# Performance work log

Hardware: AMD Instinct MI355X
Metric: run time of the kernel (lower is better)

Reference implementation:

```python
import jax, jax.numpy as jnp
import numpy as np

EMBED = 8192      # DYNAMIC(2048) + STATIC(6144)
U0, U1 = 1024, 256  # units
EGO = 3
NUM_HEAD = 6
ACTION = 2
MEAN_SCALE = 5.0
INIT_STD = 5.0
MIN_STD = 1e-4
BATCH = 8192


def setup_inputs() -> dict:
    key = jax.random.key(0)
    ks = jax.random.split(key, 10)
    s = lambda fan_in: 1.0 / np.sqrt(fan_in)
    x = jax.random.normal(ks[0], (BATCH, EMBED), dtype=jnp.float32)
    # command head index in [0, 6) == RoadOption.value - 1
    command = jax.random.randint(ks[1], (BATCH,), 0, NUM_HEAD, dtype=jnp.int32)
    ego_state = jax.random.normal(ks[2], (BATCH, EGO), dtype=jnp.float32)
    # shared trunk fc: Linear(EMBED -> U0)
    fc_W = jax.random.uniform(ks[3], (EMBED, U0), jnp.float32, -s(EMBED), s(EMBED))
    fc_b = jax.random.uniform(ks[4], (U0,), jnp.float32, -s(EMBED), s(EMBED))
    # per-head MLP: Linear(U0+EGO -> U1) -> ReLU -> Linear(U1 -> 2*ACTION)
    cin = U0 + EGO
    W1 = jax.random.uniform(ks[5], (NUM_HEAD, cin, U1), jnp.float32, -s(cin), s(cin))
    b1 = jax.random.uniform(ks[6], (NUM_HEAD, U1), jnp.float32, -s(cin), s(cin))
    W2 = jax.random.uniform(ks[7], (NUM_HEAD, U1, 2 * ACTION), jnp.float32, -s(U1), s(U1))
    b2 = jax.random.uniform(ks[8], (NUM_HEAD, 2 * ACTION), jnp.float32, -s(U1), s(U1))
    return {"x": x, "command": command, "ego_state": ego_state,
            "fc_W": fc_W, "fc_b": fc_b, "W1": W1, "b1": b1, "W2": W2, "b2": b2}


def reference(x, command, ego_state, fc_W, fc_b, W1, b1, W2, b2):
    # shared trunk: Linear + ReLU, then concat ego state -> [B, U0+EGO]
    h = jax.nn.relu(x @ fc_W + fc_b)
    h = jnp.concatenate([h, ego_state], axis=-1)
    # routed heads: compute all 6 small heads densely, then select per sample
    # (faithful math; an optimized kernel would gather->grouped GEMM->scatter)
    h1 = jax.nn.relu(jnp.einsum('bi,hio->bho', h, W1) + b1)          # [B, H, U1]
    h2 = jnp.einsum('bhi,hio->bho', h1, W2) + b2                      # [B, H, 2A]
    sel = jnp.take_along_axis(h2, command[:, None, None].astype(jnp.int32), axis=1)
    out = sel[:, 0, :]                                                # [B, 2A]
    mean, std = jnp.split(out, 2, axis=-1)
    mean = MEAN_SCALE * jnp.tanh(mean / MEAN_SCALE)
    raw_init_std = np.float32(np.log(np.exp(INIT_STD) - 1.0))
    std = jax.nn.softplus(std + raw_init_std) + MIN_STD
    # distribution parameters (pre TanhBijector Normal params)
    return jnp.concatenate([mean, std], axis=-1)
```

## Files before the change

### kernel.cpp

```cpp
#include <hip/hip_runtime.h>
#include <stdint.h>

typedef short bf16x8 __attribute__((ext_vector_type(8)));
typedef float f32x4 __attribute__((ext_vector_type(4)));

#define BATCH 8192
#define EMBED 8192
#define U0    1024
#define U1    256
#define NHEAD 6

__device__ __forceinline__ unsigned short f2bf(float f) {
  union { float f; unsigned int u; } v; v.f = f;
  unsigned int u = v.u;
  unsigned int r = u + 0x7FFFu + ((u >> 16) & 1u);
  return (unsigned short)(r >> 16);
}
__device__ __forceinline__ void async_copy16(const void* g, void* l) {
  __builtin_amdgcn_global_load_lds((const __attribute__((address_space(1))) void*)g,
                                   (__attribute__((address_space(3))) void*)l, 16, 0, 0);
}

__global__ void transpose_cvt_kernel(const float* __restrict__ in, unsigned short* __restrict__ out,
                                     int R, int C, long in_z, long out_z) {
  __shared__ unsigned short tile[64][65];
  const float* inp = in + (long)blockIdx.z * in_z;
  unsigned short* outp = out + (long)blockIdx.z * out_z;
  int r0 = blockIdx.x * 64;
  int c0 = blockIdx.y * 64;
  int lc = threadIdx.x & 63;
  int lr = threadIdx.x >> 6;
#pragma unroll
  for (int i = 0; i < 16; i++) {
    int r = lr + i * 4;
    tile[r][lc] = f2bf(inp[(long)(r0 + r) * C + (c0 + lc)]);
  }
  __syncthreads();
#pragma unroll
  for (int i = 0; i < 16; i++) {
    int c = lr + i * 4;
    outp[(long)(c0 + c) * R + (r0 + lc)] = tile[lc][c];
  }
}

__global__ void bucket_kernel(const int* __restrict__ cmd, int* __restrict__ idxlist,
                              int* __restrict__ meta) {
  __shared__ int cnt[NHEAD], cur[NHEAD], off[NHEAD + 1];
  int tid = threadIdx.x;
  if (tid < NHEAD) cnt[tid] = 0;
  __syncthreads();
  for (int b = tid; b < BATCH; b += blockDim.x) atomicAdd(&cnt[cmd[b]], 1);
  __syncthreads();
  if (tid == 0) {
    int s = 0;
    for (int h2 = 0; h2 < NHEAD; h2++) { off[h2] = s; s += cnt[h2]; }
    off[NHEAD] = s;
  }
  __syncthreads();
  if (tid < NHEAD) cur[tid] = off[tid];
  if (tid <= NHEAD) meta[tid] = off[tid];
  __syncthreads();
  for (int b = tid; b < BATCH; b += blockDim.x) {
    int p = atomicAdd(&cur[cmd[b]], 1);
    idxlist[p] = b;
  }
}

__global__ __launch_bounds__(256) void gemm_kernel(const float* __restrict__ x,
                                                   const unsigned short* __restrict__ wt,
                                                   float* __restrict__ pbuf) {
  __shared__ uint4 As[1024];
  __shared__ uint4 Bs[1024];
  int tid  = threadIdx.x;
  int lane = tid & 63;
  int wave = tid >> 6;
  int wm = wave >> 1, wn = wave & 1;

  int f = blockIdx.x;
  int xcd = f & 7;
  int idx = f >> 3;
  int kh  = idx >> 6;
  int sub = idx & 63;
  int by = xcd * 8 + (sub >> 3);
  int bx = sub & 7;
  int m0 = by * 128;
  int n0 = bx * 128;
  int l15 = lane & 15, lq = lane >> 4;

  long asrc[4], bsrc[4];
#pragma unroll
  for (int j = 0; j < 4; j++) {
    int c = wave * 4 + j;
    int cwm = c >> 3, cks = (c >> 2) & 1, cmi = c & 3;
    int kofs = cks * 32 + lq * 8;
    asrc[j] = (long)(m0 + cwm * 64 + cmi * 16 + l15) * EMBED + kofs;
    bsrc[j] = (long)(n0 + cwm * 64 + cmi * 16 + l15) * EMBED + kofs;
  }

  f32x4 zero = {0.f, 0.f, 0.f, 0.f};
  f32x4 acc[4][4];
#pragma unroll
  for (int mi = 0; mi < 4; mi++)
#pragma unroll
    for (int ni = 0; ni < 4; ni++) acc[mi][ni] = zero;

  const int kbeg = kh * 4096;
  for (int k0 = kbeg; k0 < kbeg + 4096; k0 += 64) {
    __syncthreads();
    float4 a0[4], a1[4];
#pragma unroll
    for (int j = 0; j < 4; j++) {
      const float* p = x + asrc[j] + k0;
      a0[j] = *(const float4*)p;
      a1[j] = *(const float4*)(p + 4);
    }
#pragma unroll
    for (int j = 0; j < 4; j++) {
      int c = wave * 4 + j;
      async_copy16(wt + bsrc[j] + k0, &Bs[c * 64 + lane]);
    }
#pragma unroll
    for (int j = 0; j < 4; j++) {
      int c = wave * 4 + j;
      unsigned int q0, q1, q2, q3;
      asm("v_cvt_pk_bf16_f32 %0, %1, %2" : "=v"(q0) : "v"(a0[j].x), "v"(a0[j].y));
      asm("v_cvt_pk_bf16_f32 %0, %1, %2" : "=v"(q1) : "v"(a0[j].z), "v"(a0[j].w));
      asm("v_cvt_pk_bf16_f32 %0, %1, %2" : "=v"(q2) : "v"(a1[j].x), "v"(a1[j].y));
      asm("v_cvt_pk_bf16_f32 %0, %1, %2" : "=v"(q3) : "v"(a1[j].z), "v"(a1[j].w));
      uint4 r; r.x = q0; r.y = q1; r.z = q2; r.w = q3;
      As[c * 64 + lane] = r;
    }
    __syncthreads();
#pragma unroll
    for (int ks = 0; ks < 2; ks++) {
      bf16x8 af[4], bfr[4];
#pragma unroll
      for (int mi = 0; mi < 4; mi++) af[mi] = *(const bf16x8*)&As[((wm * 2 + ks) * 4 + mi) * 64 + lane];
#pragma unroll
      for (int ni = 0; ni < 4; ni++) bfr[ni] = *(const bf16x8*)&Bs[((wn * 2 + ks) * 4 + ni) * 64 + lane];
#pragma unroll
      for (int mi = 0; mi < 4; mi++)
#pragma unroll
        for (int ni = 0; ni < 4; ni++)
          acc[mi][ni] = __builtin_amdgcn_mfma_f32_16x16x32_bf16(af[mi], bfr[ni], acc[mi][ni], 0, 0, 0);
    }
  }

  float* p = pbuf + (long)kh * (8192L * 1024);
#pragma unroll
  for (int ni = 0; ni < 4; ni++) {
    int col = n0 + wn * 64 + ni * 16 + l15;
#pragma unroll
    for (int mi = 0; mi < 4; mi++) {
      int rbase = m0 + wm * 64 + mi * 16 + lq * 4;
#pragma unroll
      for (int r = 0; r < 4; r++) {
        p[(long)(rbase + r) * U0 + col] = acc[mi][ni][r];
      }
    }
  }
}

__global__ __launch_bounds__(256) void reduce_kernel(const float* __restrict__ pbuf,
                                                     const float* __restrict__ fc_b,
                                                     unsigned short* __restrict__ h) {
  long i = ((long)blockIdx.x * 256 + threadIdx.x) * 8;
  const float* P1 = pbuf + 8192L * 1024;
  float4 a0 = *(const float4*)(pbuf + i);
  float4 a1 = *(const float4*)(pbuf + i + 4);
  float4 c0 = *(const float4*)(P1 + i);
  float4 c1 = *(const float4*)(P1 + i + 4);
  int cb = (int)(i & (U0 - 1));
  float4 b0 = *(const float4*)(fc_b + cb);
  float4 b1 = *(const float4*)(fc_b + cb + 4);
  float v[8];
  v[0] = a0.x + c0.x + b0.x; v[1] = a0.y + c0.y + b0.y;
  v[2] = a0.z + c0.z + b0.z; v[3] = a0.w + c0.w + b0.w;
  v[4] = a1.x + c1.x + b1.x; v[5] = a1.y + c1.y + b1.y;
  v[6] = a1.z + c1.z + b1.z; v[7] = a1.w + c1.w + b1.w;
  uint4 r;
  unsigned int q[4];
#pragma unroll
  for (int j = 0; j < 4; j++) {
    float lo = v[2 * j]     > 0.f ? v[2 * j]     : 0.f;
    float hi = v[2 * j + 1] > 0.f ? v[2 * j + 1] : 0.f;
    q[j] = (unsigned int)f2bf(lo) | ((unsigned int)f2bf(hi) << 16);
  }
  r.x = q[0]; r.y = q[1]; r.z = q[2]; r.w = q[3];
  *(uint4*)(h + i) = r;
}

__global__ __launch_bounds__(256) void head_kernel(const unsigned short* __restrict__ h,
                                                   const unsigned short* __restrict__ w1t,
                                                   const float* __restrict__ W1,
                                                   const float* __restrict__ b1,
                                                   const float* __restrict__ W2,
                                                   const float* __restrict__ b2,
                                                   const float* __restrict__ ego,
                                                   const int* __restrict__ idxlist,
                                                   const int* __restrict__ meta,
                                                   float* __restrict__ out) {
  int hd = blockIdx.y;
  int off = meta[hd];
  int cnt = meta[hd + 1] - off;
  int t0 = blockIdx.x * 32;
  if (t0 >= cnt) return;

  __shared__ int ridx[32];
  __shared__ float h1s[32][257];
  __shared__ float w2s[1024];
  int tid = threadIdx.x;
  if (tid < 32) {
    int i = t0 + tid;
    ridx[tid] = idxlist[off + (i < cnt ? i : 0)];
  }
  *(float4*)&w2s[tid * 4] = *(const float4*)(W2 + (long)hd * 1024 + tid * 4);
  __syncthreads();

  int lane = tid & 63, wave = tid >> 6;
  int l15 = lane & 15, lq = lane >> 4;

  long abase[2];
#pragma unroll
  for (int mi = 0; mi < 2; mi++) abase[mi] = (long)ridx[mi * 16 + l15] * U0 + lq * 8;
  long bbase[4];
#pragma unroll
  for (int ni = 0; ni < 4; ni++)
    bbase[ni] = (long)(hd * 256 + wave * 64 + ni * 16 + l15) * 1024 + lq * 8;

  f32x4 zero = {0.f, 0.f, 0.f, 0.f};
  f32x4 acc[2][4];
#pragma unroll
  for (int mi = 0; mi < 2; mi++)
#pragma unroll
    for (int ni = 0; ni < 4; ni++) acc[mi][ni] = zero;

#pragma unroll 2
  for (int k0 = 0; k0 < 1024; k0 += 32) {
    bf16x8 af[2], bfr[4];
#pragma unroll
    for (int mi = 0; mi < 2; mi++) af[mi] = *(const bf16x8*)(h + abase[mi] + k0);
#pragma unroll
    for (int ni = 0; ni < 4; ni++) bfr[ni] = *(const bf16x8*)(w1t + bbase[ni] + k0);
#pragma unroll
    for (int mi = 0; mi < 2; mi++)
#pragma unroll
      for (int ni = 0; ni < 4; ni++)
        acc[mi][ni] = __builtin_amdgcn_mfma_f32_16x16x32_bf16(af[mi], bfr[ni], acc[mi][ni], 0, 0, 0);
  }

  const float* W1e = W1 + (long)hd * 1027 * 256 + (long)1024 * 256;
#pragma unroll
  for (int mi = 0; mi < 2; mi++)
#pragma unroll
    for (int r = 0; r < 4; r++) {
      int rl = mi * 16 + lq * 4 + r;
      int b = ridx[rl];
      float e0 = ego[b * 3 + 0], e1 = ego[b * 3 + 1], e2 = ego[b * 3 + 2];
#pragma unroll
      for (int ni = 0; ni < 4; ni++) {
        int col = wave * 64 + ni * 16 + l15;
        float v = acc[mi][ni][r] + b1[hd * 256 + col]
                + e0 * W1e[col] + e1 * W1e[256 + col] + e2 * W1e[512 + col];
        h1s[rl][col] = v > 0.f ? v : 0.f;
      }
    }
  __syncthreads();

  if (tid < 128) {
    int t = tid >> 2, o2 = tid & 3;
    if (t0 + t < cnt) {
      float s0 = 0.f, s1 = 0.f, s2 = 0.f, s3 = 0.f;
#pragma unroll 4
      for (int i = 0; i < 256; i += 4) {
        s0 += h1s[t][i + 0] * w2s[(i + 0) * 4 + o2];
        s1 += h1s[t][i + 1] * w2s[(i + 1) * 4 + o2];
        s2 += h1s[t][i + 2] * w2s[(i + 2) * 4 + o2];
        s3 += h1s[t][i + 3] * w2s[(i + 3) * 4 + o2];
      }
      float sum = b2[hd * 4 + o2] + ((s0 + s1) + (s2 + s3));
      int b = ridx[t];
      float res;
      if (o2 < 2) {
        res = 5.0f * tanhf(sum * 0.2f);
      } else {
        float z = sum + 4.99323838f;
        res = (z > 20.f ? z : log1pf(expf(z))) + 1e-4f;
      }
      out[b * 4 + o2] = res;
    }
  }
}

extern "C" void kernel_launch(void* const* d_in, const int* in_sizes, int n_in,
                              void* d_out, int out_size, void* d_ws, size_t ws_size,
                              hipStream_t stream) {
  const float* x   = (const float*)d_in[0];
  const int*   cmd = (const int*)d_in[1];
  const float* ego = (const float*)d_in[2];
  const float* fcW = (const float*)d_in[3];
  const float* fcb = (const float*)d_in[4];
  const float* W1  = (const float*)d_in[5];
  const float* b1  = (const float*)d_in[6];
  const float* W2  = (const float*)d_in[7];
  const float* b2  = (const float*)d_in[8];
  float* out = (float*)d_out;

  char* ws = (char*)d_ws;
  float* pbuf          = (float*)(ws);
  unsigned short* wt   = (unsigned short*)(ws + 67108864);
  unsigned short* hbuf = (unsigned short*)(ws + 83886080);
  unsigned short* w1t  = (unsigned short*)(ws + 100663296);
  int* idxlist         = (int*)(ws + 103809024);
  int* meta            = (int*)(ws + 103841792);

  hipLaunchKernelGGL(transpose_cvt_kernel, dim3(128, 16, 1), dim3(256), 0, stream,
                     fcW, wt, 8192, 1024, 0L, 0L);
  hipLaunchKernelGGL(transpose_cvt_kernel, dim3(16, 4, 6), dim3(256), 0, stream,
                     W1, w1t, 1024, 256, (long)1027 * 256, (long)256 * 1024);
  hipLaunchKernelGGL(bucket_kernel, dim3(1), dim3(1024), 0, stream, cmd, idxlist, meta);
  hipLaunchKernelGGL(gemm_kernel, dim3(1024), dim3(256), 0, stream, x, wt, pbuf);
  hipLaunchKernelGGL(reduce_kernel, dim3(4096), dim3(256), 0, stream, pbuf, fcb, hbuf);
  hipLaunchKernelGGL(head_kernel, dim3(256, 6), dim3(256), 0, stream,
                     hbuf, w1t, W1, b1, W2, b2, ego, idxlist, meta, out);
}
```

Before: 788.6 us.

## Pre-convert x to bf16, drop split-K, fuse bias+ReLU epilogue into GEMM

Adds a separate pass that converts x to bf16 so the GEMM can load both operands into shared memory with async global-to-LDS copies. The split-K partial buffer and the reduce kernel are removed: each of 512 blocks of 512 threads covers the full K and applies bias, ReLU and bf16 packing in its epilogue. The bucket kernel now uses wave ballots to batch the shared-memory atomics. This trades an extra 256MB read plus 128MB write for the x conversion, and fewer blocks with twice the K loop, against removing the fp32 partial-sum traffic and the in-loop conversions.

```diff
diff --git a/kernel.cpp b/kernel.cpp
--- a/kernel.cpp
+++ b/kernel.cpp
@@ -16,9 +16,22 @@
   unsigned int r = u + 0x7FFFu + ((u >> 16) & 1u);
   return (unsigned short)(r >> 16);
 }
+__device__ __forceinline__ unsigned int pk2(float lo, float hi) {
+  return (unsigned int)f2bf(lo) | ((unsigned int)f2bf(hi) << 16);
+}
 __device__ __forceinline__ void async_copy16(const void* g, void* l) {
   __builtin_amdgcn_global_load_lds((const __attribute__((address_space(1))) void*)g,
                                    (__attribute__((address_space(3))) void*)l, 16, 0, 0);
+}
+
+__global__ void cvt_x_kernel(const float* __restrict__ x, unsigned short* __restrict__ xb) {
+  long i = ((long)blockIdx.x * 256 + threadIdx.x) * 8;
+  float4 a = *(const float4*)(x + i);
+  float4 b = *(const float4*)(x + i + 4);
+  uint4 r;
+  r.x = pk2(a.x, a.y); r.y = pk2(a.z, a.w);
+  r.z = pk2(b.x, b.y); r.w = pk2(b.z, b.w);
+  *(uint4*)(xb + i) = r;
 }
 
 __global__ void transpose_cvt_kernel(const float* __restrict__ in, unsigned short* __restrict__ out,
@@ -47,9 +60,17 @@
                               int* __restrict__ meta) {
   __shared__ int cnt[NHEAD], cur[NHEAD], off[NHEAD + 1];
   int tid = threadIdx.x;
+  int lane = tid & 63, wave = tid >> 6;
   if (tid < NHEAD) cnt[tid] = 0;
   __syncthreads();
-  for (int b = tid; b < BATCH; b += blockDim.x) atomicAdd(&cnt[cmd[b]], 1);
+  for (int base = wave * 64; base < BATCH; base += 1024) {
+    int c = cmd[base + lane];
+#pragma unroll
+    for (int h2 = 0; h2 < NHEAD; h2++) {
+      unsigned long long m = __ballot(c == h2);
+      if (lane == 0 && m) atomicAdd(&cnt[h2], __popcll(m));
+    }
+  }
   __syncthreads();
   if (tid == 0) {
     int s = 0;
@@ -60,134 +81,103 @@
   if (tid < NHEAD) cur[tid] = off[tid];
   if (tid <= NHEAD) meta[tid] = off[tid];
   __syncthreads();
-  for (int b = tid; b < BATCH; b += blockDim.x) {
-    int p = atomicAdd(&cur[cmd[b]], 1);
-    idxlist[p] = b;
-  }
-}
-
-__global__ __launch_bounds__(256) void gemm_kernel(const float* __restrict__ x,
+  for (int base = wave * 64; base < BATCH; base += 1024) {
+    int b = base + lane;
+    int c = cmd[b];
+    int pos = 0;
+#pragma unroll
+    for (int h2 = 0; h2 < NHEAD; h2++) {
+      unsigned long long m = __ballot(c == h2);
+      if (m) {
+        int leader = (int)(__ffsll((unsigned long long)m) - 1);
+        int wbase = 0;
+        if (lane == leader) wbase = atomicAdd(&cur[h2], __popcll(m));
+        wbase = __shfl(wbase, leader);
+        if (c == h2) pos = wbase + __popcll(m & ((1ULL << lane) - 1ULL));
+      }
+    }
+    idxlist[pos] = b;
+  }
+}
+
+__global__ __launch_bounds__(512) void gemm_kernel(const unsigned short* __restrict__ xb,
                                                    const unsigned short* __restrict__ wt,
-                                                   float* __restrict__ pbuf) {
+                                                   const float* __restrict__ fc_b,
+                                                   unsigned short* __restrict__ h) {
   __shared__ uint4 As[1024];
   __shared__ uint4 Bs[1024];
   int tid  = threadIdx.x;
   int lane = tid & 63;
   int wave = tid >> 6;
-  int wm = wave >> 1, wn = wave & 1;
+  int wm = wave >> 1;
+  int wn = wave & 1;
 
   int f = blockIdx.x;
   int xcd = f & 7;
   int idx = f >> 3;
-  int kh  = idx >> 6;
-  int sub = idx & 63;
-  int by = xcd * 8 + (sub >> 3);
-  int bx = sub & 7;
+  int by = xcd * 8 + (idx >> 3);
+  int bx = idx & 7;
   int m0 = by * 128;
   int n0 = bx * 128;
   int l15 = lane & 15, lq = lane >> 4;
 
-  long asrc[4], bsrc[4];
-#pragma unroll
-  for (int j = 0; j < 4; j++) {
-    int c = wave * 4 + j;
-    int cwm = c >> 3, cks = (c >> 2) & 1, cmi = c & 3;
-    int kofs = cks * 32 + lq * 8;
-    asrc[j] = (long)(m0 + cwm * 64 + cmi * 16 + l15) * EMBED + kofs;
-    bsrc[j] = (long)(n0 + cwm * 64 + cmi * 16 + l15) * EMBED + kofs;
+  long asrc[2], bsrc[2];
+#pragma unroll
+  for (int j = 0; j < 2; j++) {
+    int ca = wave * 2 + j;
+    int cwm = ca >> 2, cka = (ca >> 1) & 1, cmi = ca & 1;
+    asrc[j] = (long)(m0 + cwm * 32 + cmi * 16 + l15) * EMBED + cka * 32 + lq * 8;
+    int cb = wave * 2 + j;
+    int cwn = cb >> 3, ckb = (cb >> 2) & 1, cni = cb & 3;
+    bsrc[j] = (long)(n0 + cwn * 64 + cni * 16 + l15) * EMBED + ckb * 32 + lq * 8;
   }
 
   f32x4 zero = {0.f, 0.f, 0.f, 0.f};
-  f32x4 acc[4][4];
-#pragma unroll
-  for (int mi = 0; mi < 4; mi++)
+  f32x4 acc[2][4];
+#pragma unroll
+  for (int mi = 0; mi < 2; mi++)
 #pragma unroll
     for (int ni = 0; ni < 4; ni++) acc[mi][ni] = zero;
 
-  const int kbeg = kh * 4096;
-  for (int k0 = kbeg; k0 < kbeg + 4096; k0 += 64) {
+  for (int k0 = 0; k0 < EMBED; k0 += 64) {
     __syncthreads();
-    float4 a0[4], a1[4];
-#pragma unroll
-    for (int j = 0; j < 4; j++) {
-      const float* p = x + asrc[j] + k0;
-      a0[j] = *(const float4*)p;
-      a1[j] = *(const float4*)(p + 4);
-    }
-#pragma unroll
-    for (int j = 0; j < 4; j++) {
-      int c = wave * 4 + j;
+#pragma unroll
+    for (int j = 0; j < 2; j++) {
+      int c = wave * 2 + j;
+      async_copy16(xb + asrc[j] + k0, &As[c * 64 + lane]);
       async_copy16(wt + bsrc[j] + k0, &Bs[c * 64 + lane]);
     }
-#pragma unroll
-    for (int j = 0; j < 4; j++) {
-      int c = wave * 4 + j;
-      unsigned int q0, q1, q2, q3;
-      asm("v_cvt_pk_bf16_f32 %0, %1, %2" : "=v"(q0) : "v"(a0[j].x), "v"(a0[j].y));
-      asm("v_cvt_pk_bf16_f32 %0, %1, %2" : "=v"(q1) : "v"(a0[j].z), "v"(a0[j].w));
-      asm("v_cvt_pk_bf16_f32 %0, %1, %2" : "=v"(q2) : "v"(a1[j].x), "v"(a1[j].y));
-      asm("v_cvt_pk_bf16_f32 %0, %1, %2" : "=v"(q3) : "v"(a1[j].z), "v"(a1[j].w));
-      uint4 r; r.x = q0; r.y = q1; r.z = q2; r.w = q3;
-      As[c * 64 + lane] = r;
-    }
     __syncthreads();
 #pragma unroll
     for (int ks = 0; ks < 2; ks++) {
-      bf16x8 af[4], bfr[4];
-#pragma unroll
-      for (int mi = 0; mi < 4; mi++) af[mi] = *(const bf16x8*)&As[((wm * 2 + ks) * 4 + mi) * 64 + lane];
+      bf16x8 af[2], bfr[4];
+#pragma unroll
+      for (int mi = 0; mi < 2; mi++) af[mi] = *(const bf16x8*)&As[((wm * 2 + ks) * 2 + mi) * 64 + lane];
 #pragma unroll
       for (int ni = 0; ni < 4; ni++) bfr[ni] = *(const bf16x8*)&Bs[((wn * 2 + ks) * 4 + ni) * 64 + lane];
 #pragma unroll
-      for (int mi = 0; mi < 4; mi++)
+      for (int mi = 0; mi < 2; mi++)
 #pragma unroll
         for (int ni = 0; ni < 4; ni++)
           acc[mi][ni] = __builtin_amdgcn_mfma_f32_16x16x32_bf16(af[mi], bfr[ni], acc[mi][ni], 0, 0, 0);
     }
   }
 
-  float* p = pbuf + (long)kh * (8192L * 1024);
 #pragma unroll
   for (int ni = 0; ni < 4; ni++) {
     int col = n0 + wn * 64 + ni * 16 + l15;
-#pragma unroll
-    for (int mi = 0; mi < 4; mi++) {
-      int rbase = m0 + wm * 64 + mi * 16 + lq * 4;
+    float bias = fc_b[col];
+#pragma unroll
+    for (int mi = 0; mi < 2; mi++) {
+      int rbase = m0 + wm * 32 + mi * 16 + lq * 4;
 #pragma unroll
       for (int r = 0; r < 4; r++) {
-        p[(long)(rbase + r) * U0 + col] = acc[mi][ni][r];
-      }
-    }
-  }
-}
-
-__global__ __launch_bounds__(256) void reduce_kernel(const float* __restrict__ pbuf,
-                                                     const float* __restrict__ fc_b,
-                                                     unsigned short* __restrict__ h) {
-  long i = ((long)blockIdx.x * 256 + threadIdx.x) * 8;
-  const float* P1 = pbuf + 8192L * 1024;
-  float4 a0 = *(const float4*)(pbuf + i);
-  float4 a1 = *(const float4*)(pbuf + i + 4);
-  float4 c0 = *(const float4*)(P1 + i);
-  float4 c1 = *(const float4*)(P1 + i + 4);
-  int cb = (int)(i & (U0 - 1));
-  float4 b0 = *(const float4*)(fc_b + cb);
-  float4 b1 = *(const float4*)(fc_b + cb + 4);
-  float v[8];
-  v[0] = a0.x + c0.x + b0.x; v[1] = a0.y + c0.y + b0.y;
-  v[2] = a0.z + c0.z + b0.z; v[3] = a0.w + c0.w + b0.w;
-  v[4] = a1.x + c1.x + b1.x; v[5] = a1.y + c1.y + b1.y;
-  v[6] = a1.z + c1.z + b1.z; v[7] = a1.w + c1.w + b1.w;
-  uint4 r;
-  unsigned int q[4];
-#pragma unroll
-  for (int j = 0; j < 4; j++) {
-    float lo = v[2 * j]     > 0.f ? v[2 * j]     : 0.f;
-    float hi = v[2 * j + 1] > 0.f ? v[2 * j + 1] : 0.f;
-    q[j] = (unsigned int)f2bf(lo) | ((unsigned int)f2bf(hi) << 16);
-  }
-  r.x = q[0]; r.y = q[1]; r.z = q[2]; r.w = q[3];
-  *(uint4*)(h + i) = r;
+        float v = acc[mi][ni][r] + bias;
+        v = v > 0.f ? v : 0.f;
+        h[(long)(rbase + r) * U0 + col] = f2bf(v);
+      }
+    }
+  }
 }
 
 __global__ __launch_bounds__(256) void head_kernel(const unsigned short* __restrict__ h,
@@ -307,20 +297,20 @@
   float* out = (float*)d_out;
 
   char* ws = (char*)d_ws;
-  float* pbuf          = (float*)(ws);
-  unsigned short* wt   = (unsigned short*)(ws + 67108864);
-  unsigned short* hbuf = (unsigned short*)(ws + 83886080);
-  unsigned short* w1t  = (unsigned short*)(ws + 100663296);
-  int* idxlist         = (int*)(ws + 103809024);
-  int* meta            = (int*)(ws + 103841792);
-
+  unsigned short* xb   = (unsigned short*)(ws);
+  unsigned short* wt   = (unsigned short*)(ws + 134217728);
+  unsigned short* hbuf = (unsigned short*)(ws + 150994944);
+  unsigned short* w1t  = (unsigned short*)(ws + 167772160);
+  int* idxlist         = (int*)(ws + 170917888);
+  int* meta            = (int*)(ws + 170950656);
+
+  hipLaunchKernelGGL(cvt_x_kernel, dim3(32768), dim3(256), 0, stream, x, xb);
   hipLaunchKernelGGL(transpose_cvt_kernel, dim3(128, 16, 1), dim3(256), 0, stream,
                      fcW, wt, 8192, 1024, 0L, 0L);
   hipLaunchKernelGGL(transpose_cvt_kernel, dim3(16, 4, 6), dim3(256), 0, stream,
                      W1, w1t, 1024, 256, (long)1027 * 256, (long)256 * 1024);
   hipLaunchKernelGGL(bucket_kernel, dim3(1), dim3(1024), 0, stream, cmd, idxlist, meta);
-  hipLaunchKernelGGL(gemm_kernel, dim3(1024), dim3(256), 0, stream, x, wt, pbuf);
-  hipLaunchKernelGGL(reduce_kernel, dim3(4096), dim3(256), 0, stream, pbuf, fcb, hbuf);
+  hipLaunchKernelGGL(gemm_kernel, dim3(512), dim3(512), 0, stream, xb, wt, fcb, hbuf);
   hipLaunchKernelGGL(head_kernel, dim3(256, 6), dim3(256), 0, stream,
                      hbuf, w1t, W1, b1, W2, b2, ego, idxlist, meta, out);
 }
```

New measurement: 755.3 us. -4.2%, faster.
